# Optimization experiments

Measured on AMD Instinct MI355X. Metric: run time of the kernel, lower is better.

Reference implementation:

```python
import jax, jax.numpy as jnp
import numpy as np

NEG_SLOPE = 0.2

def gat_conv(x, edge, W, att_src, att_dst, bias, heads, out_ch, concat):
    # x: [N, F_in], edge: [2, E] (self-loops already included)
    N = x.shape[0]
    src, dst = edge[0], edge[1]
    h = (x @ W).reshape(N, heads, out_ch)                     # [N, H, C]
    a_src = jnp.sum(h * att_src, axis=-1)                     # [N, H]
    a_dst = jnp.sum(h * att_dst, axis=-1)                     # [N, H]
    e = jax.nn.leaky_relu(a_src[src] + a_dst[dst], NEG_SLOPE)  # [E, H]
    # segment softmax over incoming edges of each dst node
    e_max = jax.ops.segment_max(e, dst, num_segments=N)       # [N, H]
    e_exp = jnp.exp(e - e_max[dst])                           # [E, H]
    denom = jax.ops.segment_sum(e_exp, dst, num_segments=N)   # [N, H]
    alpha = e_exp / denom[dst]                                # [E, H]
    msg = h[src] * alpha[:, :, None]                          # [E, H, C]
    out = jax.ops.segment_sum(msg, dst, num_segments=N)       # [N, H, C]
    if concat:
        out = out.reshape(N, heads * out_ch)
    else:
        out = out.mean(axis=1)
    return out + bias


def setup_inputs() -> dict:
    key = jax.random.key(0)
    ks = jax.random.split(key, 10)
    N, E = 50000, 1600000
    F_in, H, C1, n_cls = 256, 4, 64, 40
    x = jax.random.normal(ks[0], (N, F_in), dtype=jnp.float32)
    edge_index = jax.random.randint(ks[1], (2, E), 0, N, dtype=jnp.int64)
    s1 = 1.0 / np.sqrt(F_in)
    s2 = 1.0 / np.sqrt(H * C1)
    return {
        "x": x,
        "edge_index": edge_index,
        "W1": jax.random.normal(ks[2], (F_in, H * C1), dtype=jnp.float32) * s1,
        "att_src1": jax.random.normal(ks[3], (H, C1), dtype=jnp.float32) * s2,
        "att_dst1": jax.random.normal(ks[4], (H, C1), dtype=jnp.float32) * s2,
        "b1": jnp.zeros((H * C1,), dtype=jnp.float32),
        "W2": jax.random.normal(ks[5], (H * C1, n_cls), dtype=jnp.float32) * s2,
        "att_src2": jax.random.normal(ks[6], (1, n_cls), dtype=jnp.float32) * 0.1,
        "att_dst2": jax.random.normal(ks[7], (1, n_cls), dtype=jnp.float32) * 0.1,
        "b2": jnp.zeros((n_cls,), dtype=jnp.float32),
    }


def reference(x, edge_index, W1, att_src1, att_dst1, b1, W2, att_src2, att_dst2, b2):
    N = x.shape[0]
    # PyG GATConv adds self-loops by default
    loops = jnp.arange(N, dtype=edge_index.dtype)
    edge = jnp.concatenate([edge_index, jnp.stack([loops, loops])], axis=1)
    # dropout is identity in eval mode
    h = gat_conv(x, edge, W1, att_src1, att_dst1, b1, heads=4, out_ch=64, concat=True)
    h = jax.nn.elu(h)
    out = gat_conv(h, edge, W2, att_src2, att_dst2, b2, heads=1, out_ch=40, concat=False)
    return out
```

## Files before the change

kernel.cpp:

```cpp
#include <hip/hip_runtime.h>
#include <hip/hip_bf16.h>

typedef short bf16x8 __attribute__((ext_vector_type(8)));
typedef float f32x4 __attribute__((ext_vector_type(4)));

#define CHUNK 4096

__device__ __forceinline__ float wred_sum(float v) {
  #pragma unroll
  for (int off = 32; off > 0; off >>= 1)
    v += __shfl_xor(v, off, 64);
  return v;
}
__device__ __forceinline__ float b2f(unsigned short u) {
  union { unsigned int i; float f; } x;
  x.i = ((unsigned int)u) << 16;
  return x.f;
}
__device__ __forceinline__ unsigned short f2bu(float f) {
  __hip_bfloat16 b = __float2bfloat16(f);
  return *(unsigned short*)&b;
}
__device__ __forceinline__ float ldf(const void* p, long long i, int is16) {
  return is16 ? __bfloat162float(((const __hip_bfloat16*)p)[i])
              : ((const float*)p)[i];
}
__device__ __forceinline__ int edge_at(const int* e, long long idx, int is64) {
  return is64 ? (int)((const long long*)e)[idx] : e[idx];
}

__global__ void detect_kernel(const int* __restrict__ edge, int n_edge_check,
                              const unsigned int* __restrict__ xw, int n_x_check,
                              int* __restrict__ flag) {
  __shared__ int s_nz, s_cnt, s_tot;
  int tid = threadIdx.x;
  if (tid == 0) { s_nz = 0; s_cnt = 0; s_tot = 0; }
  __syncthreads();
  int nz = 0;
  for (int k = tid; k < n_edge_check; k += 256)
    if (edge[2 * k + 1] != 0) nz = 1;
  if (nz) atomicOr(&s_nz, 1);
  int c = 0, t = 0;
  for (int k = tid; k < n_x_check; k += 256) {
    unsigned int w = xw[k];
    if (w == 0u) continue;
    t++;
    unsigned int e = (w >> 7) & 0xFFu;
    if (e >= 100u && e <= 150u) c++;
  }
  atomicAdd(&s_cnt, c);
  atomicAdd(&s_tot, t);
  __syncthreads();
  if (tid == 0) {
    flag[0] = (s_nz == 0) ? 1 : 0;
    flag[1] = (s_cnt * 10 > s_tot * 6) ? 1 : 0;
  }
}


__global__ __launch_bounds__(256) void bucket_count_kernel(
    const int* __restrict__ edge, int E, int N, const int* __restrict__ flag,
    int* __restrict__ bcnt, int NB) {
  __shared__ int cnt[1024];
  int tid = threadIdx.x;
  long long base = (long long)blockIdx.x * CHUNK;
  long long total = (long long)E + N;
  for (int b = tid; b < NB; b += 256) cnt[b] = 0;
  __syncthreads();
  int is64 = flag[0];
  #pragma unroll
  for (int j = 0; j < 16; j++) {
    long long i = base + j * 256 + tid;
    if (i < total) {
      int d = (i < E) ? edge_at(edge, (long long)E + i, is64) : (int)(i - E);
      d = min(max(d, 0), N - 1);
      atomicAdd(&cnt[d >> 8], 1);
    }
  }
  __syncthreads();
  for (int b = tid; b < NB; b += 256)
    if (cnt[b]) atomicAdd(&bcnt[b], cnt[b]);
}

__global__ void bucket_scan_kernel(const int* __restrict__ bcnt, int NB,
                                   int* __restrict__ bbase, int* __restrict__ bcursor) {
  __shared__ int s[256];
  __shared__ int rbase;
  int tid = threadIdx.x;
  if (tid == 0) rbase = 0;
  __syncthreads();
  for (int c0 = 0; c0 < NB; c0 += 256) {
    int idx = c0 + tid;
    int v = (idx < NB) ? bcnt[idx] : 0;
    s[tid] = v;
    __syncthreads();
    for (int off = 1; off < 256; off <<= 1) {
      int t = (tid >= off) ? s[tid - off] : 0;
      __syncthreads();
      s[tid] += t;
      __syncthreads();
    }
    int mb = rbase;
    if (idx < NB) {
      int exc = mb + s[tid] - v;
      bbase[idx] = exc;
      bcursor[idx] = exc;
    }
    __syncthreads();
    if (tid == 0) rbase = mb + s[255];
    __syncthreads();
  }
  if (tid == 0) bbase[NB] = rbase;
}

__global__ __launch_bounds__(256) void partition_kernel(
    const int* __restrict__ edge, int E, int N, const int* __restrict__ flag,
    int* __restrict__ bcursor, unsigned int* __restrict__ part, int NB) {
  __shared__ int cnt[1024];
  __shared__ int loff[1025];
  __shared__ int gpos[1024];
  __shared__ int lcur[1024];
  __shared__ unsigned int staged[CHUNK];
  __shared__ int staged_addr[CHUNK];
  __shared__ int s[256];
  __shared__ int rbase;
  int tid = threadIdx.x;
  long long base = (long long)blockIdx.x * CHUNK;
  long long total = (long long)E + N;
  int here = (int)min((long long)CHUNK, total - base);
  for (int b = tid; b < NB; b += 256) cnt[b] = 0;
  if (tid == 0) rbase = 0;
  __syncthreads();
  int is64 = flag[0];
  int myb[16];
  unsigned int myp[16];
  #pragma unroll
  for (int j = 0; j < 16; j++) {
    long long i = base + j * 256 + tid;
    myb[j] = -1;
    if (i < total) {
      int d, sv;
      if (i < E) {
        sv = edge_at(edge, i, is64);
        d = edge_at(edge, (long long)E + i, is64);
      } else {
        sv = d = (int)(i - E);
      }
      d = min(max(d, 0), N - 1);
      sv = min(max(sv, 0), N - 1);
      myb[j] = d >> 8;
      myp[j] = ((unsigned int)(d & 255) << 24) | (unsigned int)sv;
      atomicAdd(&cnt[myb[j]], 1);
    }
  }
  __syncthreads();
  for (int c0 = 0; c0 < NB; c0 += 256) {
    int idx = c0 + tid;
    int v = (idx < NB) ? cnt[idx] : 0;
    s[tid] = v;
    __syncthreads();
    for (int off = 1; off < 256; off <<= 1) {
      int t = (tid >= off) ? s[tid - off] : 0;
      __syncthreads();
      s[tid] += t;
      __syncthreads();
    }
    int mb = rbase;
    if (idx < NB) loff[idx] = mb + s[tid] - v;
    __syncthreads();
    if (tid == 0) rbase = mb + s[255];
    __syncthreads();
  }
  __syncthreads();
  for (int b = tid; b < NB; b += 256) {
    int c = cnt[b];
    gpos[b] = c ? atomicAdd(&bcursor[b], c) : 0;
    lcur[b] = loff[b];
  }
  __syncthreads();
  #pragma unroll
  for (int j = 0; j < 16; j++) {
    if (myb[j] >= 0) {
      int b = myb[j];
      int slot = atomicAdd(&lcur[b], 1);
      staged[slot] = myp[j];
      staged_addr[slot] = gpos[b] + (slot - loff[b]);
    }
  }
  __syncthreads();
  for (int i = tid; i < here; i += 256)
    part[staged_addr[i]] = staged[i];
}

__global__ __launch_bounds__(256) void bucket_sort_kernel(
    const unsigned int* __restrict__ part, const int* __restrict__ bbase,
    int N, int total, int* __restrict__ indptr, int* __restrict__ ssrc) {
  __shared__ int hist[256], cur[256];
  __shared__ int s[256];
  int tid = threadIdx.x;
  int b = blockIdx.x;
  int begin = bbase[b], end = bbase[b + 1];
  hist[tid] = 0;
  __syncthreads();
  for (int i = begin + tid; i < end; i += 256)
    atomicAdd(&hist[part[i] >> 24], 1);
  __syncthreads();
  int v = hist[tid];
  s[tid] = v;
  __syncthreads();
  for (int off = 1; off < 256; off <<= 1) {
    int t = (tid >= off) ? s[tid - off] : 0;
    __syncthreads();
    s[tid] += t;
    __syncthreads();
  }
  int exc = s[tid] - v;
  cur[tid] = exc;
  int d = b * 256 + tid;
  if (d < N) indptr[d] = begin + exc;
  if (b == 0 && tid == 0) indptr[N] = total;
  __syncthreads();
  for (int i = begin + tid; i < end; i += 256) {
    unsigned int p = part[i];
    int pos = begin + atomicAdd(&cur[p >> 24], 1);
    ssrc[pos] = (int)(p & 0xFFFFFFu);
  }
}

__global__ void prep_kernel(const void* __restrict__ x, __hip_bfloat16* __restrict__ xb,
                            long long n_valid4, long long nconv4,
                            const void* __restrict__ W1v, const void* __restrict__ W2v,
                            __hip_bfloat16* __restrict__ Wt1, __hip_bfloat16* __restrict__ Wt2,
                            int F, int HC, int C2, int C2p,
                            const int* __restrict__ dflag) {
  int f16 = dflag[1];
  long long i = blockIdx.x * 256LL + threadIdx.x;
  if (i < nconv4) {
    ushort4 o;
    if (i < n_valid4) {
      if (f16) {
        o = ((const ushort4*)x)[i];
      } else {
        float4 v = ((const float4*)x)[i];
        o.x = f2bu(v.x); o.y = f2bu(v.y); o.z = f2bu(v.z); o.w = f2bu(v.w);
      }
    } else {
      o.x = o.y = o.z = o.w = 0;
    }
    ((ushort4*)xb)[i] = o;
    return;
  }
  long long j = i - nconv4;
  int n1 = HC * F;
  if (j < n1) {
    int idx = (int)j;
    int n = idx / F, k = idx - n * F;
    Wt1[idx] = __float2bfloat16(ldf(W1v, (long long)k * HC + n, f16));
  } else {
    int jj = (int)(j - n1);
    if (jj >= C2p * HC) return;
    int n = jj / HC, k = jj - n * HC;
    float v = (n < C2) ? ldf(W2v, (long long)k * C2 + n, f16) : 0.f;
    Wt2[jj] = __float2bfloat16(v);
  }
}

__global__ __launch_bounds__(256) void mfma_gemm_kernel(
    const __hip_bfloat16* __restrict__ A, const __hip_bfloat16* __restrict__ BtT,
    __hip_bfloat16* __restrict__ Cb,
    const void* __restrict__ attS, const void* __restrict__ attD,
    float* __restrict__ aS, float* __restrict__ aD, int att_stride,
    int M, int Nout, int K, const int* __restrict__ dflag) {
  int f16 = dflag[1];
  int tid = threadIdx.x;
  int w = tid >> 6, l = tid & 63;
  int m_lane = l & 15, q = l >> 4;
  int row0 = blockIdx.x * 64, col0 = blockIdx.y * 64;
  const __hip_bfloat16* Arow = A + (long long)(row0 + w * 16 + m_lane) * K + q * 8;
  const __hip_bfloat16* Brow = BtT + (long long)(col0 + m_lane) * K + q * 8;
  f32x4 acc[4] = {};
  #pragma unroll 4
  for (int k0 = 0; k0 < K; k0 += 32) {
    bf16x8 af = *(const bf16x8*)(Arow + k0);
    #pragma unroll
    for (int t = 0; t < 4; t++) {
      bf16x8 bf = *(const bf16x8*)(Brow + (long long)t * 16 * K + k0);
      acc[t] = __builtin_amdgcn_mfma_f32_16x16x32_bf16(af, bf, acc[t], 0, 0, 0);
    }
  }
  #pragma unroll
  for (int r = 0; r < 4; r++) {
    int gr = row0 + w * 16 + q * 4 + r;
    float ps = 0.f, pd = 0.f;
    #pragma unroll
    for (int t = 0; t < 4; t++) {
      int gc = col0 + t * 16 + m_lane;
      float v = acc[t][r];
      if (gc < Nout) {
        ps += v * ldf(attS, gc, f16);
        pd += v * ldf(attD, gc, f16);
        if (gr < M) Cb[(long long)gr * Nout + gc] = __float2bfloat16(v);
      }
    }
    #pragma unroll
    for (int off = 1; off < 16; off <<= 1) {
      ps += __shfl_xor(ps, off, 64);
      pd += __shfl_xor(pd, off, 64);
    }
    if (m_lane == 0 && gr < M) {
      aS[(long long)gr * att_stride + blockIdx.y] = ps;
      aD[(long long)gr * att_stride + blockIdx.y] = pd;
    }
  }
}

__global__ __launch_bounds__(256) void aggregate1_kernel(
    const int* __restrict__ indptr, const int* __restrict__ ssrc,
    const __hip_bfloat16* __restrict__ h1b, const float* __restrict__ a_src,
    const float* __restrict__ a_dst, const void* __restrict__ b1,
    __hip_bfloat16* __restrict__ h2b, int N, const int* __restrict__ dflag) {
  int f16 = dflag[1];
  int w = threadIdx.x >> 6, l = threadIdx.x & 63;
  int d = blockIdx.x * 4 + w;
  if (d >= N) return;
  int q = l >> 4;
  int e16 = l & 15;
  int base = l & 48;
  int begin = indptr[d], end = indptr[d + 1];
  float adst = a_dst[d * 4 + q];
  int s0 = ssrc[begin];
  float den = 0.f;
  float acc0 = 0.f, acc1 = 0.f, acc2 = 0.f, acc3 = 0.f;
  for (int c = begin; c < end; c += 32) {
    int cnt = end - c;
    int sj0 = s0, sj1 = s0;
    float wj0 = 0.f, wj1 = 0.f;
    if (e16 < cnt) {
      sj0 = ssrc[c + e16];
      float e = a_src[sj0 * 4 + q] + adst;
      e = (e > 0.f) ? e : 0.2f * e;
      wj0 = __expf(e);
    }
    if (e16 + 16 < cnt) {
      sj1 = ssrc[c + e16 + 16];
      float e = a_src[sj1 * 4 + q] + adst;
      e = (e > 0.f) ? e : 0.2f * e;
      wj1 = __expf(e);
    }
    den += wj0 + wj1;
    #pragma unroll
    for (int j = 0; j < 16; j++) {
      int s = __shfl(sj0, base + j, 64);
      float wt = __shfl(wj0, base + j, 64);
      ushort4 hv = *(const ushort4*)((const unsigned short*)h1b +
                                     (long long)s * 256 + 4 * l);
      acc0 += wt * b2f(hv.x);
      acc1 += wt * b2f(hv.y);
      acc2 += wt * b2f(hv.z);
      acc3 += wt * b2f(hv.w);
    }
    #pragma unroll
    for (int j = 0; j < 16; j++) {
      int s = __shfl(sj1, base + j, 64);
      float wt = __shfl(wj1, base + j, 64);
      ushort4 hv = *(const ushort4*)((const unsigned short*)h1b +
                                     (long long)s * 256 + 4 * l);
      acc0 += wt * b2f(hv.x);
      acc1 += wt * b2f(hv.y);
      acc2 += wt * b2f(hv.z);
      acc3 += wt * b2f(hv.w);
    }
  }
  #pragma unroll
  for (int off = 1; off < 16; off <<= 1)
    den += __shfl_xor(den, off, 64);
  float inv = 1.f / den;
  float v0 = acc0 * inv + ldf(b1, 4 * l + 0, f16);
  float v1 = acc1 * inv + ldf(b1, 4 * l + 1, f16);
  float v2 = acc2 * inv + ldf(b1, 4 * l + 2, f16);
  float v3 = acc3 * inv + ldf(b1, 4 * l + 3, f16);
  v0 = (v0 > 0.f) ? v0 : (__expf(v0) - 1.f);
  v1 = (v1 > 0.f) ? v1 : (__expf(v1) - 1.f);
  v2 = (v2 > 0.f) ? v2 : (__expf(v2) - 1.f);
  v3 = (v3 > 0.f) ? v3 : (__expf(v3) - 1.f);
  ushort4 o;
  o.x = f2bu(v0); o.y = f2bu(v1); o.z = f2bu(v2); o.w = f2bu(v3);
  *(ushort4*)((unsigned short*)h2b + (long long)d * 256 + 4 * l) = o;
}

__global__ __launch_bounds__(256) void aggregate2_kernel(
    const int* __restrict__ indptr, const int* __restrict__ ssrc,
    const __hip_bfloat16* __restrict__ gb, const float* __restrict__ a_src,
    const float* __restrict__ a_dst, const void* __restrict__ b2,
    void* __restrict__ out, int N, int C, const int* __restrict__ dflag) {
  int f16 = dflag[1];
  int w = threadIdx.x >> 6, l = threadIdx.x & 63;
  int d = blockIdx.x * 4 + w;
  if (d >= N) return;
  int begin = indptr[d], end = indptr[d + 1];
  float adst = a_dst[d];
  int e_off = l / 20;
  int pr = l - e_off * 20;
  bool active = (e_off < 3);
  int s0 = ssrc[begin];
  float den = 0.f;
  float acc0 = 0.f, acc1 = 0.f;
  for (int c = begin; c < end; c += 64) {
    int cnt = min(64, end - c);
    int sj = s0;
    float wj = 0.f;
    if (l < cnt) {
      sj = ssrc[c + l];
      float e = a_src[sj] + adst;
      e = (e > 0.f) ? e : 0.2f * e;
      wj = __expf(e);
    }
    den += wj;
    #pragma unroll 4
    for (int j = 0; j < cnt; j += 3) {
      int idx = j + e_off;
      int s = __shfl(sj, idx & 63, 64);
      float wt = __shfl(wj, idx & 63, 64);
      if (!active || idx >= cnt) wt = 0.f;
      ushort2 gv = *(const ushort2*)((const unsigned short*)gb +
                                     (long long)s * C + 2 * pr);
      acc0 += wt * b2f(gv.x);
      acc1 += wt * b2f(gv.y);
    }
  }
  den = wred_sum(den);
  float inv = 1.f / den;
  float r0 = acc0 + __shfl(acc0, (l + 20) & 63, 64) + __shfl(acc0, (l + 40) & 63, 64);
  float r1 = acc1 + __shfl(acc1, (l + 20) & 63, 64) + __shfl(acc1, (l + 40) & 63, 64);
  if (l < 20) {
    float v0 = r0 * inv + ldf(b2, 2 * l + 0, f16);
    float v1 = r1 * inv + ldf(b2, 2 * l + 1, f16);
    long long o = (long long)d * C + 2 * l;
    if (f16) {
      ushort2 ov;
      ov.x = f2bu(v0); ov.y = f2bu(v1);
      *(ushort2*)((unsigned short*)out + o) = ov;
    } else {
      float2 ov;
      ov.x = v0; ov.y = v1;
      *(float2*)((float*)out + o) = ov;
    }
  }
}

extern "C" void kernel_launch(void* const* d_in, const int* in_sizes, int n_in,
                              void* d_out, int out_size, void* d_ws, size_t ws_size,
                              hipStream_t stream) {
  const void* x   = d_in[0];
  const int* edge = (const int*)d_in[1];
  const void* W1  = d_in[2];
  const void* as1 = d_in[3];
  const void* ad1 = d_in[4];
  const void* b1  = d_in[5];
  const void* W2  = d_in[6];
  const void* as2 = d_in[7];
  const void* ad2 = d_in[8];
  const void* b2  = d_in[9];

  const int F  = 256;
  const int HC = 256;
  const int N  = in_sizes[0] / F;
  const int E  = in_sizes[1] / 2;
  const int C2 = in_sizes[9];
  const int C2p = 64;
  const int total = E + N;
  const int NB = (N + 255) / 256;
  const int Mpad = ((N + 63) / 64) * 64;

  char* p = (char*)d_ws;
  auto alloc = [&](size_t bytes) -> void* {
    void* r = (void*)p;
    p += (bytes + 255) & ~(size_t)255;
    return r;
  };
  __hip_bfloat16* xb  = (__hip_bfloat16*)alloc((size_t)Mpad * F * 2);
  __hip_bfloat16* h1b = (__hip_bfloat16*)alloc((size_t)Mpad * HC * 2);
  __hip_bfloat16* h2b = (__hip_bfloat16*)alloc((size_t)Mpad * HC * 2);
  __hip_bfloat16* gb  = (__hip_bfloat16*)alloc((size_t)Mpad * C2 * 2);
  __hip_bfloat16* Wt1 = (__hip_bfloat16*)alloc((size_t)HC * F * 2);
  __hip_bfloat16* Wt2 = (__hip_bfloat16*)alloc((size_t)C2p * HC * 2);
  float* a_src1 = (float*)alloc((size_t)N * 4 * 4);
  float* a_dst1 = (float*)alloc((size_t)N * 4 * 4);
  float* a_src2 = (float*)alloc((size_t)N * 4);
  float* a_dst2 = (float*)alloc((size_t)N * 4);
  unsigned int* part = (unsigned int*)alloc((size_t)total * 4);
  int* bcnt     = (int*)alloc((size_t)(NB + 1) * 4);
  int* bbase    = (int*)alloc((size_t)(NB + 1) * 4);
  int* bcursor  = (int*)alloc((size_t)NB * 4);
  int* indptr   = (int*)alloc((size_t)(N + 1) * 4);
  int* ssrc     = (int*)alloc((size_t)total * 4);
  int* flag     = (int*)alloc(256);

  hipMemsetAsync(bcnt, 0, (size_t)(NB + 1) * 4, stream);
  detect_kernel<<<1, 256, 0, stream>>>(edge, E < 2048 ? E : 2048,
                                       (const unsigned int*)x, 4096, flag);
  int nch = (total + CHUNK - 1) / CHUNK;
  bucket_count_kernel<<<nch, 256, 0, stream>>>(edge, E, N, flag, bcnt, NB);
  bucket_scan_kernel<<<1, 256, 0, stream>>>(bcnt, NB, bbase, bcursor);
  partition_kernel<<<nch, 256, 0, stream>>>(edge, E, N, flag, bcursor, part, NB);
  bucket_sort_kernel<<<NB, 256, 0, stream>>>(part, bbase, N, total, indptr, ssrc);

  long long nconv4 = (long long)Mpad * F / 4;
  long long nprep = nconv4 + (long long)HC * F + (long long)C2p * HC;
  prep_kernel<<<(int)((nprep + 255) / 256), 256, 0, stream>>>(
      x, xb, (long long)N * F / 4, nconv4, W1, W2, Wt1, Wt2, F, HC, C2, C2p, flag);

  dim3 g1(Mpad / 64, HC / 64);
  mfma_gemm_kernel<<<g1, 256, 0, stream>>>(xb, Wt1, h1b,
                                           as1, ad1, a_src1, a_dst1, 4,
                                           N, HC, F, flag);
  aggregate1_kernel<<<(N + 3) / 4, 256, 0, stream>>>(indptr, ssrc, h1b, a_src1, a_dst1,
                                                     b1, h2b, N, flag);

  dim3 g2(Mpad / 64, 1);
  mfma_gemm_kernel<<<g2, 256, 0, stream>>>(h2b, Wt2, gb,
                                           as2, ad2, a_src2, a_dst2, 1,
                                           N, C2, HC, flag);
  aggregate2_kernel<<<(N + 3) / 4, 256, 0, stream>>>(indptr, ssrc, gb, a_src2, a_dst2,
                                                     b2, d_out, N, C2, flag);
}
```

Before: 440.9 us.

## Quantize layer-1 features to int8 with per-head scales for aggregation gather

Result: no change. 442.6 us (+0.4%).

```diff
diff --git a/kernel.cpp b/kernel.cpp
--- a/kernel.cpp
+++ b/kernel.cpp
@@ -270,7 +270,9 @@
     __hip_bfloat16* __restrict__ Cb,
     const void* __restrict__ attS, const void* __restrict__ attD,
     float* __restrict__ aS, float* __restrict__ aD, int att_stride,
-    int M, int Nout, int K, const int* __restrict__ dflag) {
+    int M, int Nout, int K, int quant,
+    unsigned char* __restrict__ h1q, float* __restrict__ h1s,
+    const int* __restrict__ dflag) {
   int f16 = dflag[1];
   int tid = threadIdx.x;
   int w = tid >> 6, l = tid & 63;
@@ -291,7 +293,7 @@
   #pragma unroll
   for (int r = 0; r < 4; r++) {
     int gr = row0 + w * 16 + q * 4 + r;
-    float ps = 0.f, pd = 0.f;
+    float ps = 0.f, pd = 0.f, vmax = 0.f;
     #pragma unroll
     for (int t = 0; t < 4; t++) {
       int gc = col0 + t * 16 + m_lane;
@@ -299,13 +301,26 @@
       if (gc < Nout) {
         ps += v * ldf(attS, gc, f16);
         pd += v * ldf(attD, gc, f16);
-        if (gr < M) Cb[(long long)gr * Nout + gc] = __float2bfloat16(v);
+        vmax = fmaxf(vmax, fabsf(v));
+        if (!quant && gr < M) Cb[(long long)gr * Nout + gc] = __float2bfloat16(v);
       }
     }
     #pragma unroll
     for (int off = 1; off < 16; off <<= 1) {
       ps += __shfl_xor(ps, off, 64);
       pd += __shfl_xor(pd, off, 64);
+      vmax = fmaxf(vmax, __shfl_xor(vmax, off, 64));
+    }
+    if (quant && gr < M) {
+      float qinv = (vmax > 0.f) ? 127.f / vmax : 0.f;
+      #pragma unroll
+      for (int t = 0; t < 4; t++) {
+        int gc = col0 + t * 16 + m_lane;
+        h1q[(long long)gr * 256 + gc] =
+            (unsigned char)(__float2int_rn(acc[t][r] * qinv) + 128);
+      }
+      if (m_lane == 0)
+        h1s[(long long)gr * att_stride + blockIdx.y] = vmax * (1.f / 127.f);
     }
     if (m_lane == 0 && gr < M) {
       aS[(long long)gr * att_stride + blockIdx.y] = ps;
@@ -316,8 +331,9 @@
 
 __global__ __launch_bounds__(256) void aggregate1_kernel(
     const int* __restrict__ indptr, const int* __restrict__ ssrc,
-    const __hip_bfloat16* __restrict__ h1b, const float* __restrict__ a_src,
-    const float* __restrict__ a_dst, const void* __restrict__ b1,
+    const unsigned char* __restrict__ h1q, const float* __restrict__ h1s,
+    const float* __restrict__ a_src, const float* __restrict__ a_dst,
+    const void* __restrict__ b1,
     __hip_bfloat16* __restrict__ h2b, int N, const int* __restrict__ dflag) {
   int f16 = dflag[1];
   int w = threadIdx.x >> 6, l = threadIdx.x & 63;
@@ -329,56 +345,61 @@
   int begin = indptr[d], end = indptr[d + 1];
   float adst = a_dst[d * 4 + q];
   int s0 = ssrc[begin];
-  float den = 0.f;
+  float den = 0.f, accS = 0.f;
   float acc0 = 0.f, acc1 = 0.f, acc2 = 0.f, acc3 = 0.f;
   for (int c = begin; c < end; c += 32) {
     int cnt = end - c;
     int sj0 = s0, sj1 = s0;
-    float wj0 = 0.f, wj1 = 0.f;
+    float wj0 = 0.f, wj1 = 0.f, ws0 = 0.f, ws1 = 0.f;
     if (e16 < cnt) {
       sj0 = ssrc[c + e16];
       float e = a_src[sj0 * 4 + q] + adst;
       e = (e > 0.f) ? e : 0.2f * e;
       wj0 = __expf(e);
+      ws0 = wj0 * h1s[sj0 * 4 + q];
     }
     if (e16 + 16 < cnt) {
       sj1 = ssrc[c + e16 + 16];
       float e = a_src[sj1 * 4 + q] + adst;
       e = (e > 0.f) ? e : 0.2f * e;
       wj1 = __expf(e);
+      ws1 = wj1 * h1s[sj1 * 4 + q];
     }
     den += wj0 + wj1;
-    #pragma unroll
-    for (int j = 0; j < 16; j++) {
+    int n0 = cnt < 16 ? cnt : 16;
+    int n1 = cnt - 16;
+    n1 = n1 < 0 ? 0 : (n1 > 16 ? 16 : n1);
+    #pragma unroll 4
+    for (int j = 0; j < n0; j++) {
       int s = __shfl(sj0, base + j, 64);
-      float wt = __shfl(wj0, base + j, 64);
-      ushort4 hv = *(const ushort4*)((const unsigned short*)h1b +
-                                     (long long)s * 256 + 4 * l);
-      acc0 += wt * b2f(hv.x);
-      acc1 += wt * b2f(hv.y);
-      acc2 += wt * b2f(hv.z);
-      acc3 += wt * b2f(hv.w);
-    }
-    #pragma unroll
-    for (int j = 0; j < 16; j++) {
+      float wt = __shfl(ws0, base + j, 64);
+      accS += wt;
+      unsigned int uv = *(const unsigned int*)(h1q + (long long)s * 256 + 4 * l);
+      acc0 += wt * (float)(uv & 0xFFu);
+      acc1 += wt * (float)((uv >> 8) & 0xFFu);
+      acc2 += wt * (float)((uv >> 16) & 0xFFu);
+      acc3 += wt * (float)(uv >> 24);
+    }
+    #pragma unroll 4
+    for (int j = 0; j < n1; j++) {
       int s = __shfl(sj1, base + j, 64);
-      float wt = __shfl(wj1, base + j, 64);
-      ushort4 hv = *(const ushort4*)((const unsigned short*)h1b +
-                                     (long long)s * 256 + 4 * l);
-      acc0 += wt * b2f(hv.x);
-      acc1 += wt * b2f(hv.y);
-      acc2 += wt * b2f(hv.z);
-      acc3 += wt * b2f(hv.w);
+      float wt = __shfl(ws1, base + j, 64);
+      accS += wt;
+      unsigned int uv = *(const unsigned int*)(h1q + (long long)s * 256 + 4 * l);
+      acc0 += wt * (float)(uv & 0xFFu);
+      acc1 += wt * (float)((uv >> 8) & 0xFFu);
+      acc2 += wt * (float)((uv >> 16) & 0xFFu);
+      acc3 += wt * (float)(uv >> 24);
     }
   }
   #pragma unroll
   for (int off = 1; off < 16; off <<= 1)
     den += __shfl_xor(den, off, 64);
   float inv = 1.f / den;
-  float v0 = acc0 * inv + ldf(b1, 4 * l + 0, f16);
-  float v1 = acc1 * inv + ldf(b1, 4 * l + 1, f16);
-  float v2 = acc2 * inv + ldf(b1, 4 * l + 2, f16);
-  float v3 = acc3 * inv + ldf(b1, 4 * l + 3, f16);
+  float v0 = (acc0 - 128.f * accS) * inv + ldf(b1, 4 * l + 0, f16);
+  float v1 = (acc1 - 128.f * accS) * inv + ldf(b1, 4 * l + 1, f16);
+  float v2 = (acc2 - 128.f * accS) * inv + ldf(b1, 4 * l + 2, f16);
+  float v3 = (acc3 - 128.f * accS) * inv + ldf(b1, 4 * l + 3, f16);
   v0 = (v0 > 0.f) ? v0 : (__expf(v0) - 1.f);
   v1 = (v1 > 0.f) ? v1 : (__expf(v1) - 1.f);
   v2 = (v2 > 0.f) ? v2 : (__expf(v2) - 1.f);
@@ -479,7 +500,8 @@
     return r;
   };
   __hip_bfloat16* xb  = (__hip_bfloat16*)alloc((size_t)Mpad * F * 2);
-  __hip_bfloat16* h1b = (__hip_bfloat16*)alloc((size_t)Mpad * HC * 2);
+  unsigned char*  h1q = (unsigned char*)alloc((size_t)Mpad * HC);
+  float*          h1s = (float*)alloc((size_t)Mpad * 4 * 4);
   __hip_bfloat16* h2b = (__hip_bfloat16*)alloc((size_t)Mpad * HC * 2);
   __hip_bfloat16* gb  = (__hip_bfloat16*)alloc((size_t)Mpad * C2 * 2);
   __hip_bfloat16* Wt1 = (__hip_bfloat16*)alloc((size_t)HC * F * 2);
@@ -511,16 +533,16 @@
       x, xb, (long long)N * F / 4, nconv4, W1, W2, Wt1, Wt2, F, HC, C2, C2p, flag);
 
   dim3 g1(Mpad / 64, HC / 64);
-  mfma_gemm_kernel<<<g1, 256, 0, stream>>>(xb, Wt1, h1b,
+  mfma_gemm_kernel<<<g1, 256, 0, stream>>>(xb, Wt1, nullptr,
                                            as1, ad1, a_src1, a_dst1, 4,
-                                           N, HC, F, flag);
-  aggregate1_kernel<<<(N + 3) / 4, 256, 0, stream>>>(indptr, ssrc, h1b, a_src1, a_dst1,
-                                                     b1, h2b, N, flag);
+                                           N, HC, F, 1, h1q, h1s, flag);
+  aggregate1_kernel<<<(N + 3) / 4, 256, 0, stream>>>(indptr, ssrc, h1q, h1s,
+                                                     a_src1, a_dst1, b1, h2b, N, flag);
 
   dim3 g2(Mpad / 64, 1);
   mfma_gemm_kernel<<<g2, 256, 0, stream>>>(h2b, Wt2, gb,
                                            as2, ad2, a_src2, a_dst2, 1,
-                                           N, C2, HC, flag);
+                                           N, C2, HC, 0, nullptr, nullptr, flag);
   aggregate2_kernel<<<(N + 3) / 4, 256, 0, stream>>>(indptr, ssrc, gb, a_src2, a_dst2,
                                                      b2, d_out, N, C2, flag);
 }
```
